# Kernel optimization log

Hardware: AMD Instinct MI355X
Metric: run time of the kernel (lower is better)

## Reference

```python
import jax, jax.numpy as jnp
import numpy as np


def setup_inputs() -> dict:
    key = jax.random.key(0)
    k1, k2 = jax.random.split(key)
    B, C, N = 8, 11, 64  # batch, fragment channels, cubic voxel grid edge
    inp = jax.random.normal(k1, (B, C, N, N, N), dtype=jnp.float32)
    tar = jax.random.normal(k2, (B, C, N, N, N), dtype=jnp.float32)
    # 20 contiguous bins spanning [-4, 4]; bin_range[k] = (lo_k, hi_k)
    edges = jnp.linspace(-4.0, 4.0, 21, dtype=jnp.float32)
    bin_range = jnp.stack([edges[:-1], edges[1:]], axis=-1)  # [20, 2]
    return {"inp": inp, "tar": tar, "bin_range": bin_range}


def _bin_data(x, bin_range):
    # x: [B, C, nx, ny, nz] -> normalized histogram [B, C, K]
    B, C = x.shape[0], x.shape[1]
    nvox = x.shape[2] * x.shape[3] * x.shape[4]
    xf = x.reshape(B, C, -1)  # [B, C, nvox]

    def count_one_bin(b):  # b: [2] = (lo, hi)
        return jnp.sum((xf >= b[0]) & (xf < b[1]), axis=-1).astype(jnp.float32)

    # sequential over K bins (small, fixed) to avoid a [K,B,C,nvox] mask blowup
    counts = jax.lax.map(count_one_bin, bin_range)  # [K, B, C]
    return jnp.transpose(counts, (1, 2, 0)) / jnp.float32(nvox)


def _smooth_l1(a, b):
    # torch.nn.SmoothL1Loss default: beta=1.0, mean reduction
    d = jnp.abs(a - b)
    return jnp.mean(jnp.where(d < 1.0, 0.5 * d * d, d - 0.5))


def reference(inp, tar, bin_range):
    loss1 = _smooth_l1(inp, tar)
    loss2 = jnp.mean(jnp.abs(_bin_data(inp, bin_range) - _bin_data(tar, bin_range)))
    return 0.5 * loss1 + 0.5 * loss2
```

## Files before the change

kernel.cpp:

```cpp
#include <hip/hip_runtime.h>

#define BC 88
#define NVOX 262144
#define KBINS 20
#define SPLIT 32
#define THREADS 256
#define EPB (NVOX / SPLIT)
#define V4PT (EPB / (THREADS * 4))
#define NSUB 64
#define HSTRIDE 23
#define NBLOCKS (BC * SPLIT)

__global__ void __launch_bounds__(THREADS)
binloss_main(const float* __restrict__ inp, const float* __restrict__ tar,
             const float* __restrict__ br, int* __restrict__ g_hist,
             float* __restrict__ partials)
{
    __shared__ int   sh[NSUB * HSTRIDE];
    __shared__ float wsum[THREADS / 64];

    const int tid = threadIdx.x;
    for (int i = tid; i < NSUB * HSTRIDE; i += THREADS) sh[i] = 0;

    const float e0    = br[0];
    const float eK    = br[2 * KBINS - 1];
    const float inv_w = (float)KBINS / (eK - e0);
    const float shift = -e0 * inv_w;
    __syncthreads();

    const int bid = blockIdx.x;
    const int ch  = bid >> 5;
    const int s   = bid & (SPLIT - 1);
    const size_t base = (size_t)ch * NVOX + (size_t)s * EPB;
    const float4* ip = (const float4*)(inp + base);
    const float4* tp = (const float4*)(tar + base);

    int* myh = &sh[(tid & 63) * HSTRIDE];
    float s_lin = 0.f, s_quad = 0.f;

#pragma unroll
    for (int j = 0; j < V4PT; ++j) {
        float4 a = ip[j * THREADS + tid];
        float4 b = tp[j * THREADS + tid];
#pragma unroll
        for (int c = 0; c < 4; ++c) {
            float av = (&a.x)[c], bv = (&b.x)[c];
            float d = fabsf(av - bv);
            float m = fminf(d, 1.0f);
            s_lin += d - m;
            s_quad = __builtin_fmaf(m, m, s_quad);
            float ta = __builtin_amdgcn_fmed3f(__builtin_fmaf(av, inv_w, shift), -1.0f, (float)KBINS + 0.5f);
            float tb = __builtin_amdgcn_fmed3f(__builtin_fmaf(bv, inv_w, shift), -1.0f, (float)KBINS + 0.5f);
            int ka = (int)floorf(ta);
            int kb = (int)floorf(tb);
            atomicAdd(&myh[ka + 1], 1);
            atomicAdd(&myh[kb + 1], -1);
        }
    }

    float sl1 = s_lin + 0.5f * s_quad;
    for (int off = 32; off > 0; off >>= 1) sl1 += __shfl_down(sl1, off, 64);
    if ((tid & 63) == 0) wsum[tid >> 6] = sl1;
    __syncthreads();
    if (tid == 0) {
        float tot = 0.f;
        for (int w = 0; w < THREADS / 64; ++w) tot += wsum[w];
        partials[bid] = tot;
    }

    for (int k = 1 + tid; k <= KBINS; k += THREADS) {
        int t = 0;
#pragma unroll
        for (int h = 0; h < NSUB; ++h) t += sh[h * HSTRIDE + k];
        atomicAdd(&g_hist[ch * KBINS + (k - 1)], t);
    }
}

__global__ void __launch_bounds__(256)
binloss_final(const int* __restrict__ g_hist, const float* __restrict__ partials,
              float* __restrict__ out)
{
    __shared__ double r1[256];
    __shared__ double r2[256];
    const int tid = threadIdx.x;
    double s1 = 0.0, s2 = 0.0;
    for (int i = tid; i < NBLOCKS; i += 256) s1 += (double)partials[i];
    for (int i = tid; i < BC * KBINS; i += 256) s2 += fabs((double)g_hist[i]);
    r1[tid] = s1; r2[tid] = s2;
    __syncthreads();
    for (int off = 128; off > 0; off >>= 1) {
        if (tid < off) { r1[tid] += r1[tid + off]; r2[tid] += r2[tid + off]; }
        __syncthreads();
    }
    if (tid == 0) {
        const double ntot  = (double)BC * (double)NVOX;
        double loss1 = r1[0] / ntot;
        double loss2 = r2[0] / ((double)NVOX * (double)(BC * KBINS));
        out[0] = (float)(0.5 * loss1 + 0.5 * loss2);
    }
}

extern "C" void kernel_launch(void* const* d_in, const int* in_sizes, int n_in,
                              void* d_out, int out_size, void* d_ws, size_t ws_size,
                              hipStream_t stream) {
    const float* inp = (const float*)d_in[0];
    const float* tar = (const float*)d_in[1];
    const float* br  = (const float*)d_in[2];

    int*   g_hist   = (int*)d_ws;
    float* partials = (float*)((char*)d_ws + BC * KBINS * sizeof(int));

    hipMemsetAsync(d_ws, 0, BC * KBINS * sizeof(int), stream);

    binloss_main<<<NBLOCKS, THREADS, 0, stream>>>(inp, tar, br, g_hist, partials);
    binloss_final<<<1, 256, 0, stream>>>(g_hist, partials, (float*)d_out);
}
```

Measured before the change: 44.82 us.

## Replace LDS atomic histogram with register-resident CDF counts per edge

Each element is compared against all 21 bin edges and the results are accumulated into per-thread register counters of a cumulative count. These counters are then reduced across the wavefront with shuffles and across the block through LDS, and the final kernel differences adjacent CDF entries to recover the bins. This removes the LDS atomic traffic and the 64-way sub-histogram reduction, and it uses the actual bin edges instead of assuming uniform width. In exchange it costs about 42 compare/add operations per element pair in VALU work and adds register pressure, which may make the kernel compute-bound.

```diff
diff --git a/kernel.cpp b/kernel.cpp
--- a/kernel.cpp
+++ b/kernel.cpp
@@ -3,30 +3,27 @@
 #define BC 88
 #define NVOX 262144
 #define KBINS 20
+#define NEDGE 21
 #define SPLIT 32
 #define THREADS 256
 #define EPB (NVOX / SPLIT)
 #define V4PT (EPB / (THREADS * 4))
-#define NSUB 64
-#define HSTRIDE 23
 #define NBLOCKS (BC * SPLIT)
 
 __global__ void __launch_bounds__(THREADS)
 binloss_main(const float* __restrict__ inp, const float* __restrict__ tar,
-             const float* __restrict__ br, int* __restrict__ g_hist,
+             const float* __restrict__ br, int* __restrict__ g_cdf,
              float* __restrict__ partials)
 {
-    __shared__ int   sh[NSUB * HSTRIDE];
+    __shared__ int   s_c[THREADS / 64][NEDGE];
     __shared__ float wsum[THREADS / 64];
 
     const int tid = threadIdx.x;
-    for (int i = tid; i < NSUB * HSTRIDE; i += THREADS) sh[i] = 0;
 
-    const float e0    = br[0];
-    const float eK    = br[2 * KBINS - 1];
-    const float inv_w = (float)KBINS / (eK - e0);
-    const float shift = -e0 * inv_w;
-    __syncthreads();
+    float e[NEDGE];
+#pragma unroll
+    for (int j = 0; j < KBINS; ++j) e[j] = br[2 * j];
+    e[KBINS] = br[2 * KBINS - 1];
 
     const int bid = blockIdx.x;
     const int ch  = bid >> 5;
@@ -35,49 +32,55 @@
     const float4* ip = (const float4*)(inp + base);
     const float4* tp = (const float4*)(tar + base);
 
-    int* myh = &sh[(tid & 63) * HSTRIDE];
+    int c[NEDGE];
+#pragma unroll
+    for (int j = 0; j < NEDGE; ++j) c[j] = 0;
     float s_lin = 0.f, s_quad = 0.f;
 
 #pragma unroll
-    for (int j = 0; j < V4PT; ++j) {
-        float4 a = ip[j * THREADS + tid];
-        float4 b = tp[j * THREADS + tid];
+    for (int it = 0; it < V4PT; ++it) {
+        float4 a = ip[it * THREADS + tid];
+        float4 b = tp[it * THREADS + tid];
 #pragma unroll
-        for (int c = 0; c < 4; ++c) {
-            float av = (&a.x)[c], bv = (&b.x)[c];
+        for (int q = 0; q < 4; ++q) {
+            float av = (&a.x)[q], bv = (&b.x)[q];
             float d = fabsf(av - bv);
             float m = fminf(d, 1.0f);
             s_lin += d - m;
             s_quad = __builtin_fmaf(m, m, s_quad);
-            float ta = __builtin_amdgcn_fmed3f(__builtin_fmaf(av, inv_w, shift), -1.0f, (float)KBINS + 0.5f);
-            float tb = __builtin_amdgcn_fmed3f(__builtin_fmaf(bv, inv_w, shift), -1.0f, (float)KBINS + 0.5f);
-            int ka = (int)floorf(ta);
-            int kb = (int)floorf(tb);
-            atomicAdd(&myh[ka + 1], 1);
-            atomicAdd(&myh[kb + 1], -1);
+#pragma unroll
+            for (int j = 0; j < NEDGE; ++j) {
+                c[j] += (av < e[j]);
+                c[j] -= (bv < e[j]);
+            }
         }
     }
 
     float sl1 = s_lin + 0.5f * s_quad;
+#pragma unroll
     for (int off = 32; off > 0; off >>= 1) sl1 += __shfl_down(sl1, off, 64);
-    if ((tid & 63) == 0) wsum[tid >> 6] = sl1;
+
+    const int wv = tid >> 6, ln = tid & 63;
+#pragma unroll
+    for (int j = 0; j < NEDGE; ++j) {
+        int v = c[j];
+#pragma unroll
+        for (int off = 32; off > 0; off >>= 1) v += __shfl_down(v, off, 64);
+        if (ln == 0) s_c[wv][j] = v;
+    }
+    if (ln == 0) wsum[wv] = sl1;
     __syncthreads();
-    if (tid == 0) {
-        float tot = 0.f;
-        for (int w = 0; w < THREADS / 64; ++w) tot += wsum[w];
-        partials[bid] = tot;
-    }
 
-    for (int k = 1 + tid; k <= KBINS; k += THREADS) {
-        int t = 0;
-#pragma unroll
-        for (int h = 0; h < NSUB; ++h) t += sh[h * HSTRIDE + k];
-        atomicAdd(&g_hist[ch * KBINS + (k - 1)], t);
+    if (tid == 0)
+        partials[bid] = wsum[0] + wsum[1] + wsum[2] + wsum[3];
+    if (tid < NEDGE) {
+        int t = s_c[0][tid] + s_c[1][tid] + s_c[2][tid] + s_c[3][tid];
+        atomicAdd(&g_cdf[ch * NEDGE + tid], t);
     }
 }
 
 __global__ void __launch_bounds__(256)
-binloss_final(const int* __restrict__ g_hist, const float* __restrict__ partials,
+binloss_final(const int* __restrict__ g_cdf, const float* __restrict__ partials,
               float* __restrict__ out)
 {
     __shared__ double r1[256];
@@ -85,7 +88,11 @@
     const int tid = threadIdx.x;
     double s1 = 0.0, s2 = 0.0;
     for (int i = tid; i < NBLOCKS; i += 256) s1 += (double)partials[i];
-    for (int i = tid; i < BC * KBINS; i += 256) s2 += fabs((double)g_hist[i]);
+    for (int i = tid; i < BC * KBINS; i += 256) {
+        int ch = i / KBINS, k = i - ch * KBINS;
+        int hd = g_cdf[ch * NEDGE + k + 1] - g_cdf[ch * NEDGE + k];
+        s2 += fabs((double)hd);
+    }
     r1[tid] = s1; r2[tid] = s2;
     __syncthreads();
     for (int off = 128; off > 0; off >>= 1) {
@@ -107,11 +114,11 @@
     const float* tar = (const float*)d_in[1];
     const float* br  = (const float*)d_in[2];
 
-    int*   g_hist   = (int*)d_ws;
-    float* partials = (float*)((char*)d_ws + BC * KBINS * sizeof(int));
+    int*   g_cdf    = (int*)d_ws;
+    float* partials = (float*)((char*)d_ws + BC * NEDGE * sizeof(int));
 
-    hipMemsetAsync(d_ws, 0, BC * KBINS * sizeof(int), stream);
+    hipMemsetAsync(d_ws, 0, BC * NEDGE * sizeof(int), stream);
 
-    binloss_main<<<NBLOCKS, THREADS, 0, stream>>>(inp, tar, br, g_hist, partials);
-    binloss_final<<<1, 256, 0, stream>>>(g_hist, partials, (float*)d_out);
+    binloss_main<<<NBLOCKS, THREADS, 0, stream>>>(inp, tar, br, g_cdf, partials);
+    binloss_final<<<1, 256, 0, stream>>>(g_cdf, partials, (float*)d_out);
 }
```

Result: slower. 83.56 us (+86.4%).

## Redistribute work as fixed chunks across 2048 blocks with channel-straddling histogram flush

Applied to the files above, without the earlier changes.

Replaces the per-channel split (88×32 blocks) with 2048 blocks, each processing 11 contiguous 1024-element chunks. A block whose chunks cross a channel boundary flushes its shared histogram and starts a second pass for the next channel. It also folds the +1 bin offset into the shift so floorf is dropped, uses fmaxf(d,1) with a constant correction, parallelises the final row reduction across 80 threads, and sets an occupancy hint. The aim is a grid that better matches the CU count and cheaper inner-loop arithmetic. The cost is extra branches and syncs. Float truncation replacing floor is safe because the clamp keeps values at or above zero.

```diff
diff --git a/kernel.cpp b/kernel.cpp
--- a/kernel.cpp
+++ b/kernel.cpp
@@ -3,77 +3,107 @@
 #define BC 88
 #define NVOX 262144
 #define KBINS 20
-#define SPLIT 32
 #define THREADS 256
-#define EPB (NVOX / SPLIT)
-#define V4PT (EPB / (THREADS * 4))
+#define NBLOCKS 2048
+#define CHUNK 1024
+#define CPB 11
+#define CPC 256
+#define HSTRIDE 23
 #define NSUB 64
-#define HSTRIDE 23
-#define NBLOCKS (BC * SPLIT)
 
-__global__ void __launch_bounds__(THREADS)
+__global__ void __launch_bounds__(THREADS, 8)
 binloss_main(const float* __restrict__ inp, const float* __restrict__ tar,
              const float* __restrict__ br, int* __restrict__ g_hist,
              float* __restrict__ partials)
 {
-    __shared__ int   sh[NSUB * HSTRIDE];
+    __shared__ int   rows[NSUB * HSTRIDE];
     __shared__ float wsum[THREADS / 64];
 
     const int tid = threadIdx.x;
-    for (int i = tid; i < NSUB * HSTRIDE; i += THREADS) sh[i] = 0;
+    for (int i = tid; i < NSUB * HSTRIDE; i += THREADS) rows[i] = 0;
 
-    const float e0    = br[0];
-    const float eK    = br[2 * KBINS - 1];
-    const float inv_w = (float)KBINS / (eK - e0);
-    const float shift = -e0 * inv_w;
+    const float e0     = br[0];
+    const float eK     = br[2 * KBINS - 1];
+    const float inv_w  = (float)KBINS / (eK - e0);
+    const float shift1 = 1.0f - e0 * inv_w;
+    const float tmax   = (float)(KBINS + 1) + 0.5f;
     __syncthreads();
 
-    const int bid = blockIdx.x;
-    const int ch  = bid >> 5;
-    const int s   = bid & (SPLIT - 1);
-    const size_t base = (size_t)ch * NVOX + (size_t)s * EPB;
-    const float4* ip = (const float4*)(inp + base);
-    const float4* tp = (const float4*)(tar + base);
+    const int fc  = blockIdx.x * CPB;
+    const int ch0 = fc >> 8;
+    const int rem = fc & (CPC - 1);
+    const int n1  = (rem + CPB > CPC) ? (CPC - rem) : CPB;
 
-    int* myh = &sh[(tid & 63) * HSTRIDE];
+    const float4* ip4 = (const float4*)inp;
+    const float4* tp4 = (const float4*)tar;
+    int* myrow = &rows[(tid & 63) * HSTRIDE];
+
     float s_lin = 0.f, s_quad = 0.f;
 
+#pragma unroll 2
+    for (int c = fc; c < fc + n1; ++c) {
+        float4 a = ip4[(size_t)c * 256 + tid];
+        float4 b = tp4[(size_t)c * 256 + tid];
 #pragma unroll
-    for (int j = 0; j < V4PT; ++j) {
-        float4 a = ip[j * THREADS + tid];
-        float4 b = tp[j * THREADS + tid];
+        for (int q = 0; q < 4; ++q) {
+            float av = (&a.x)[q], bv = (&b.x)[q];
+            float d = fabsf(av - bv);
+            s_lin += fmaxf(d, 1.0f);
+            float m = fminf(d, 1.0f);
+            s_quad  = __builtin_fmaf(m, m, s_quad);
+            int sa = (int)__builtin_amdgcn_fmed3f(__builtin_fmaf(av, inv_w, shift1), 0.0f, tmax);
+            int sb = (int)__builtin_amdgcn_fmed3f(__builtin_fmaf(bv, inv_w, shift1), 0.0f, tmax);
+            atomicAdd(&myrow[sa], 1);
+            atomicAdd(&myrow[sb], -1);
+        }
+    }
+    __syncthreads();
+    if (tid < 80) {
+        int bin = tid % KBINS, qr = tid / KBINS;
+        int s = 0;
 #pragma unroll
-        for (int c = 0; c < 4; ++c) {
-            float av = (&a.x)[c], bv = (&b.x)[c];
-            float d = fabsf(av - bv);
-            float m = fminf(d, 1.0f);
-            s_lin += d - m;
-            s_quad = __builtin_fmaf(m, m, s_quad);
-            float ta = __builtin_amdgcn_fmed3f(__builtin_fmaf(av, inv_w, shift), -1.0f, (float)KBINS + 0.5f);
-            float tb = __builtin_amdgcn_fmed3f(__builtin_fmaf(bv, inv_w, shift), -1.0f, (float)KBINS + 0.5f);
-            int ka = (int)floorf(ta);
-            int kb = (int)floorf(tb);
-            atomicAdd(&myh[ka + 1], 1);
-            atomicAdd(&myh[kb + 1], -1);
+        for (int r = qr * 16; r < qr * 16 + 16; ++r) s += rows[r * HSTRIDE + 1 + bin];
+        atomicAdd(&g_hist[ch0 * KBINS + bin], s);
+    }
+
+    if (n1 < CPB) {
+        __syncthreads();
+        for (int i = tid; i < NSUB * HSTRIDE; i += THREADS) rows[i] = 0;
+        __syncthreads();
+#pragma unroll 2
+        for (int c = fc + n1; c < fc + CPB; ++c) {
+            float4 a = ip4[(size_t)c * 256 + tid];
+            float4 b = tp4[(size_t)c * 256 + tid];
+#pragma unroll
+            for (int q = 0; q < 4; ++q) {
+                float av = (&a.x)[q], bv = (&b.x)[q];
+                float d = fabsf(av - bv);
+                s_lin += fmaxf(d, 1.0f);
+                float m = fminf(d, 1.0f);
+                s_quad  = __builtin_fmaf(m, m, s_quad);
+                int sa = (int)__builtin_amdgcn_fmed3f(__builtin_fmaf(av, inv_w, shift1), 0.0f, tmax);
+                int sb = (int)__builtin_amdgcn_fmed3f(__builtin_fmaf(bv, inv_w, shift1), 0.0f, tmax);
+                atomicAdd(&myrow[sa], 1);
+                atomicAdd(&myrow[sb], -1);
+            }
+        }
+        __syncthreads();
+        if (tid < 80) {
+            int bin = tid % KBINS, qr = tid / KBINS;
+            int s = 0;
+#pragma unroll
+            for (int r = qr * 16; r < qr * 16 + 16; ++r) s += rows[r * HSTRIDE + 1 + bin];
+            atomicAdd(&g_hist[(ch0 + 1) * KBINS + bin], s);
         }
     }
 
-    float sl1 = s_lin + 0.5f * s_quad;
+    float sl1 = (s_lin - (float)(CPB * 4)) + 0.5f * s_quad;
+#pragma unroll
     for (int off = 32; off > 0; off >>= 1) sl1 += __shfl_down(sl1, off, 64);
     if ((tid & 63) == 0) wsum[tid >> 6] = sl1;
     __syncthreads();
-    if (tid == 0) {
-        float tot = 0.f;
-        for (int w = 0; w < THREADS / 64; ++w) tot += wsum[w];
-        partials[bid] = tot;
-    }
-
-    for (int k = 1 + tid; k <= KBINS; k += THREADS) {
-        int t = 0;
-#pragma unroll
-        for (int h = 0; h < NSUB; ++h) t += sh[h * HSTRIDE + k];
-        atomicAdd(&g_hist[ch * KBINS + (k - 1)], t);
-    }
+    if (tid == 0)
+        partials[blockIdx.x] = wsum[0] + wsum[1] + wsum[2] + wsum[3];
 }
 
 __global__ void __launch_bounds__(256)
```

After: 44.73 us. No clear change (-0.2%).
